# Optimization experiments

Measured on AMD Instinct MI355X. Metric: run time of the kernel, lower is better.

## Reference

```python
import jax, jax.numpy as jnp
import numpy as np

B, DIM, H, W = 32, 384, 32, 32
ORDER = 5
DIMS = [DIM // 2**i for i in range(ORDER)][::-1]  # [24,48,96,192,384]
SUM_DIMS = sum(DIMS)                               # 744 == 2*DIM - DIMS[0]
SCALE = 1.0 / 3.0
EPS = 1e-5


def setup_inputs() -> dict:
    key = jax.random.key(0)
    ks = jax.random.split(key, 32)

    def n(k, shape, s=0.02):
        return jax.random.normal(k, shape, jnp.float32) * s

    inp = {}
    inp['x'] = jax.random.normal(ks[0], (B, DIM, H, W), jnp.float32)
    # norm1: LayerNorm([dim, H, W]) -> per-element affine
    inp['ln1_w'] = jnp.ones((DIM, H, W), jnp.float32) + n(ks[1], (DIM, H, W))
    inp['ln1_b'] = n(ks[2], (DIM, H, W))
    # gnconv params
    inp['proj_in_w'] = n(ks[3], (2 * DIM, DIM))   # 1x1 conv stored as [O,C]
    inp['proj_in_b'] = n(ks[4], (2 * DIM,))
    inp['dw_w'] = n(ks[5], (SUM_DIMS, 1, 7, 7))   # depthwise 7x7
    inp['dw_b'] = n(ks[6], (SUM_DIMS,))
    for i in range(ORDER - 1):
        inp[f'pw{i}_w'] = n(ks[7 + 2 * i], (DIMS[i + 1], DIMS[i]))
        inp[f'pw{i}_b'] = n(ks[8 + 2 * i], (DIMS[i + 1],))
    inp['proj_out_w'] = n(ks[15], (DIM, DIM))
    inp['proj_out_b'] = n(ks[16], (DIM,))
    # norm2 + MLP
    inp['ln2_w'] = jnp.ones((DIM,), jnp.float32) + n(ks[17], (DIM,))
    inp['ln2_b'] = n(ks[18], (DIM,))
    inp['fc1_w'] = n(ks[19], (4 * DIM, DIM))
    inp['fc1_b'] = n(ks[20], (4 * DIM,))
    inp['fc2_w'] = n(ks[21], (DIM, 4 * DIM))
    inp['fc2_b'] = n(ks[22], (DIM,))
    # layer scales
    inp['gamma1'] = 1e-6 * jnp.ones((DIM,), jnp.float32)
    inp['gamma2'] = 1e-6 * jnp.ones((DIM,), jnp.float32)
    return inp


def _conv1x1(x, w, b):
    # x: [B,C,H,W], w: [O,C] -> [B,O,H,W]
    return jnp.einsum('bchw,oc->bohw', x, w) + b[None, :, None, None]


def _dwconv7(x, w, b):
    y = jax.lax.conv_general_dilated(
        x, w, window_strides=(1, 1), padding=[(3, 3), (3, 3)],
        dimension_numbers=('NCHW', 'OIHW', 'NCHW'),
        feature_group_count=x.shape[1])
    return y + b[None, :, None, None]


def reference(x, ln1_w, ln1_b, proj_in_w, proj_in_b, dw_w, dw_b,
              pw0_w, pw0_b, pw1_w, pw1_b, pw2_w, pw2_b, pw3_w, pw3_b,
              proj_out_w, proj_out_b, ln2_w, ln2_b,
              fc1_w, fc1_b, fc2_w, fc2_b, gamma1, gamma2):
    # ---- norm1: LayerNorm over (C,H,W) jointly ----
    mu = x.mean(axis=(1, 2, 3), keepdims=True)
    var = x.var(axis=(1, 2, 3), keepdims=True)
    h = (x - mu) * jax.lax.rsqrt(var + EPS) * ln1_w[None] + ln1_b[None]

    # ---- gnconv (recursive gated conv) ----
    fused = _conv1x1(h, proj_in_w, proj_in_b)          # [B, 2*DIM, H, W]
    pwa = fused[:, :DIMS[0]]
    abc = fused[:, DIMS[0]:]                            # [B, SUM_DIMS, H, W]
    dw = _dwconv7(abc, dw_w, dw_b) * SCALE
    dw_list = jnp.split(dw, np.cumsum(DIMS)[:-1].tolist(), axis=1)
    y = pwa * dw_list[0]
    for i, (wp, bp) in enumerate([(pw0_w, pw0_b), (pw1_w, pw1_b), (pw2_w, pw2_b), (pw3_w, pw3_b)]):
        y = _conv1x1(y, wp, bp) * dw_list[i + 1]
    y = _conv1x1(y, proj_out_w, proj_out_b)             # [B, DIM, H, W]

    x = x + gamma1[None, :, None, None] * y             # residual 1 (drop_path=0 -> identity)

    # ---- ConvNeXt-style MLP, channels-last ----
    h = jnp.transpose(x, (0, 2, 3, 1))                  # [B,H,W,C]
    mu2 = h.mean(axis=-1, keepdims=True)
    var2 = h.var(axis=-1, keepdims=True)
    h = (h - mu2) * jax.lax.rsqrt(var2 + EPS) * ln2_w + ln2_b
    h = jnp.einsum('bhwc,oc->bhwo', h, fc1_w) + fc1_b
    h = jax.nn.gelu(h, approximate=False)               # torch GELU default = erf
    h = jnp.einsum('bhwc,oc->bhwo', h, fc2_w) + fc2_b
    h = gamma2 * h
    h = jnp.transpose(h, (0, 3, 1, 2))                  # back to NCHW
    return x + h
```

## Files before the change

### kernel.cpp

```cpp
#include <hip/hip_runtime.h>
#include <math.h>

#define HW 1024
#define CDIM 384
#define NB 32
#define MTOT (NB * HW)
#define EPS 1e-5f

typedef unsigned short u16;
typedef short s8v __attribute__((ext_vector_type(8)));
typedef float f4v __attribute__((ext_vector_type(4)));

union U8 { s8v v; u16 u[8]; };

__device__ __forceinline__ float bf2f(u16 u) {
  union { float f; unsigned int i; } x; x.i = ((unsigned int)u) << 16; return x.f;
}
__device__ __forceinline__ u16 f2bf(float f) {
  union { float f; unsigned int i; } x; x.f = f;
  unsigned int r = (x.i + 0x7FFFu + ((x.i >> 16) & 1u)) >> 16;
  return (u16)r;
}
__device__ __forceinline__ float gelu_exact(float v) {
  return 0.5f * v * (1.f + erff(v * 0.70710678118654752f));
}

__device__ __forceinline__ void gload16(const u16* g, u16* l) {
  __builtin_amdgcn_global_load_lds(
      (const __attribute__((address_space(1))) unsigned int*)(unsigned long long)(const void*)g,
      (__attribute__((address_space(3))) unsigned int*)(unsigned int)(unsigned long long)(void*)l,
      16, 0, 0);
}

__global__ __launch_bounds__(256) void k_statsA(const float* __restrict__ x,
                                                float* __restrict__ part) {
  int blk = blockIdx.x;
  const float4* xb = (const float4*)(x + (size_t)blk * 12288);
  float s = 0.f, s2 = 0.f;
  for (int i = threadIdx.x; i < 3072; i += 256) {
    float4 v = xb[i];
    s += v.x + v.y + v.z + v.w;
    s2 += v.x * v.x + v.y * v.y + v.z * v.z + v.w * v.w;
  }
  __shared__ float ls[256], ls2[256];
  ls[threadIdx.x] = s; ls2[threadIdx.x] = s2;
  __syncthreads();
  for (int off = 128; off > 0; off >>= 1) {
    if (threadIdx.x < off) {
      ls[threadIdx.x] += ls[threadIdx.x + off];
      ls2[threadIdx.x] += ls2[threadIdx.x + off];
    }
    __syncthreads();
  }
  if (threadIdx.x == 0) { part[blk * 2] = ls[0]; part[blk * 2 + 1] = ls2[0]; }
}

__global__ void k_statsB(const float* __restrict__ part, float* __restrict__ stats) {
  int b = threadIdx.x;
  if (b >= 32) return;
  float s = 0.f, s2 = 0.f;
  for (int i = 0; i < 32; i++) {
    s += part[(b * 32 + i) * 2];
    s2 += part[(b * 32 + i) * 2 + 1];
  }
  const float inv_n = 1.f / (CDIM * HW);
  float m = s * inv_n;
  stats[b] = m;
  stats[32 + b] = rsqrtf(s2 * inv_n - m * m + EPS);
}

__global__ __launch_bounds__(256) void k_cvtwE(const float* __restrict__ piw,
                                               const float* __restrict__ pow_,
                                               const float* __restrict__ p0w,
                                               const float* __restrict__ p1w,
                                               const float* __restrict__ p2w,
                                               const float* __restrict__ p3w,
                                               u16* __restrict__ dst) {
  int i = blockIdx.x * 256 + threadIdx.x;
  if (i < 294912) dst[i] = f2bf(piw[i]);
  else if (i < 442368) dst[i] = f2bf(pow_[i - 294912]);
  else if (i < 443904) { int j = i - 442368, o = j >> 5, k = j & 31;
    dst[i] = (k < 24) ? f2bf(p0w[o * 24 + k]) : (u16)0; }
  else if (i < 450048) { int j = i - 443904, o = j >> 6, k = j & 63;
    dst[i] = (k < 48) ? f2bf(p1w[o * 48 + k]) : (u16)0; }
  else if (i < 468480) dst[i] = f2bf(p2w[i - 450048]);
  else dst[i] = f2bf(p3w[i - 468480]);
}

__global__ __launch_bounds__(256) void k_cvtwL(const float* __restrict__ fc1,
                                               const float* __restrict__ fc2,
                                               u16* __restrict__ dst) {
  int i = blockIdx.x * 256 + threadIdx.x;
  if (i < 589824) dst[i] = f2bf(fc1[i]);
  else dst[i] = f2bf(fc2[i - 589824]);
}

__global__ __launch_bounds__(256) void k_trln1(const float* __restrict__ x,
                                               const float* __restrict__ lnw,
                                               const float* __restrict__ lnb,
                                               const float* __restrict__ stats,
                                               u16* __restrict__ xn,
                                               u16* __restrict__ hn) {
  int pt = blockIdx.x, ct = blockIdx.y, b = blockIdx.z;
  __shared__ float xs[32][33], hs[32][33];
  float m = stats[b], rs = stats[32 + b];
  int t = threadIdx.x;
  int ci0 = t >> 5, pi = t & 31;
#pragma unroll
  for (int it = 0; it < 4; it++) {
    int ci = ci0 + it * 8;
    int c = ct * 32 + ci;
    size_t src = ((size_t)b * CDIM + c) * HW + pt * 32 + pi;
    size_t wsrc = (size_t)c * HW + pt * 32 + pi;
    float xv = x[src];
    xs[ci][pi] = xv;
    hs[ci][pi] = (xv - m) * rs * lnw[wsrc] + lnb[wsrc];
  }
  __syncthreads();
  int co = t & 31, pr0 = t >> 5;
#pragma unroll
  for (int it = 0; it < 4; it++) {
    int pr = pr0 + it * 8;
    int p = pt * 32 + pr;
    int c = ct * 32 + co;
    size_t dst = ((size_t)b * HW + p) * CDIM + c;
    xn[dst] = f2bf(xs[co][pr]);
    hn[dst] = f2bf(hs[co][pr]);
  }
}

template <int MODE>
__global__ __launch_bounds__(256)
void k_mfma(const u16* __restrict__ A, const u16* __restrict__ Wb,
            const float* __restrict__ bias, void* __restrict__ Out,
            const u16* __restrict__ gate, int gate_off,
            const u16* __restrict__ resbf, const float* __restrict__ gvec,
            int m_base, int K, int O, int OS) {
  __shared__ u16 As[4096];
  __shared__ u16 Bs[4096];
  const int t = threadIdx.x;
  const int m0 = blockIdx.x * 128, o0 = blockIdx.y * 128;
  const int w = t >> 6, l = t & 63;
  const int wm = (w >> 1) * 64, wn = (w & 1) * 64;
  const int lr = l & 15, lk = (l >> 4) * 8;

  const u16* gA = A + (size_t)(m0 + w * 32 + (l >> 2)) * K + (l & 3) * 8;
  const u16* gB = Wb + (size_t)(o0 + w * 32 + (l >> 2)) * K + (l & 3) * 8;
  u16* ldsA0 = As + w * 1024;
  u16* ldsB0 = Bs + w * 1024;

  f4v acc[4][4];
#pragma unroll
  for (int i = 0; i < 4; i++)
#pragma unroll
    for (int j = 0; j < 4; j++) acc[i][j] = {};

  for (int k0 = 0; k0 < K; k0 += 32) {
    gload16(gA + k0, ldsA0);
    gload16(gA + 16 * K + k0, ldsA0 + 512);
    gload16(gB + k0, ldsB0);
    gload16(gB + 16 * K + k0, ldsB0 + 512);
    __syncthreads();
    s8v a[4], b[4];
#pragma unroll
    for (int mi = 0; mi < 4; mi++)
      a[mi] = *(const s8v*)&As[(wm + mi * 16 + lr) * 32 + lk];
#pragma unroll
    for (int fj = 0; fj < 4; fj++)
      b[fj] = *(const s8v*)&Bs[(wn + fj * 16 + lr) * 32 + lk];
#pragma unroll
    for (int mi = 0; mi < 4; mi++)
#pragma unroll
      for (int fj = 0; fj < 4; fj++)
        acc[mi][fj] = __builtin_amdgcn_mfma_f32_16x16x32_bf16(a[mi], b[fj], acc[mi][fj], 0, 0, 0);
    __syncthreads();
  }

  const int orow = (l >> 4) * 4;
#pragma unroll
  for (int mi = 0; mi < 4; mi++) {
    int p = m0 + wm + mi * 16 + orow;
#pragma unroll
    for (int fj = 0; fj < 4; fj++) {
      int o = o0 + wn + fj * 16 + lr;
      if (MODE == 1 && o >= OS) continue;
      float bo = (MODE == 1 && o >= O) ? 0.f : bias[o];
      float gv = (MODE == 2 || MODE == 4) ? gvec[o] : 0.f;
      if (MODE == 4) {
        int gp = m_base + p;
        float4 st;
        float* stp = &st.x;
#pragma unroll
        for (int r = 0; r < 4; r++)
          stp[r] = bf2f(resbf[(size_t)(gp + r) * CDIM + o]) + gv * (acc[mi][fj][r] + bo);
        int bb = gp >> 10, hw = gp & 1023;
        *(float4*)((float*)Out + ((size_t)bb * CDIM + o) * HW + hw) = st;
      } else {
#pragma unroll
        for (int r = 0; r < 4; r++) {
          float val = acc[mi][fj][r] + bo;
          size_t rowi = (size_t)(p + r);
          if (MODE == 0) {
            ((u16*)Out)[rowi * OS + o] = f2bf(val);
          } else if (MODE == 1) {
            float g = (o < O) ? bf2f(gate[rowi * 744 + gate_off + o]) : 0.f;
            ((u16*)Out)[rowi * OS + o] = (o < O) ? f2bf(val * g) : (u16)0;
          } else if (MODE == 2) {
            size_t idx = rowi * CDIM + o;
            ((u16*)Out)[idx] = f2bf(bf2f(resbf[idx]) + gv * val);
          } else if (MODE == 3) {
            ((u16*)Out)[rowi * OS + o] = f2bf(gelu_exact(val));
          }
        }
      }
    }
  }
}

template <int MODE>
__global__ __launch_bounds__(256)
void k_mfma64(const u16* __restrict__ A, const u16* __restrict__ Wb,
              const float* __restrict__ bias, void* __restrict__ Out,
              const u16* __restrict__ gate, int gate_off,
              const u16* __restrict__ resbf, const float* __restrict__ gvec,
              int m_base, int K, int O, int OS) {
  __shared__ u16 As[4096];
  __shared__ u16 Bs[2048];
  const int t = threadIdx.x;
  const int m0 = blockIdx.x * 128, o0 = blockIdx.y * 64;
  const int w = t >> 6, l = t & 63;
  const int wm = w * 32;
  const int lr = l & 15, lk = (l >> 4) * 8;

  const u16* gA = A + (size_t)(m0 + w * 32 + (l >> 2)) * K + (l & 3) * 8;
  const u16* gB = Wb + (size_t)(o0 + w * 16 + (l >> 2)) * K + (l & 3) * 8;
  u16* ldsA0 = As + w * 1024;
  u16* ldsB0 = Bs + w * 512;

  f4v acc[2][4];
#pragma unroll
  for (int i = 0; i < 2; i++)
#pragma unroll
    for (int j = 0; j < 4; j++) acc[i][j] = {};

  for (int k0 = 0; k0 < K; k0 += 32) {
    gload16(gA + k0, ldsA0);
    gload16(gA + 16 * K + k0, ldsA0 + 512);
    gload16(gB + k0, ldsB0);
    __syncthreads();
    s8v a[2], b[4];
#pragma unroll
    for (int mi = 0; mi < 2; mi++)
      a[mi] = *(const s8v*)&As[(wm + mi * 16 + lr) * 32 + lk];
#pragma unroll
    for (int fj = 0; fj < 4; fj++)
      b[fj] = *(const s8v*)&Bs[(fj * 16 + lr) * 32 + lk];
#pragma unroll
    for (int mi = 0; mi < 2; mi++)
#pragma unroll
      for (int fj = 0; fj < 4; fj++)
        acc[mi][fj] = __builtin_amdgcn_mfma_f32_16x16x32_bf16(a[mi], b[fj], acc[mi][fj], 0, 0, 0);
    __syncthreads();
  }

  const int orow = (l >> 4) * 4;
#pragma unroll
  for (int mi = 0; mi < 2; mi++) {
    int p = m0 + wm + mi * 16 + orow;
#pragma unroll
    for (int fj = 0; fj < 4; fj++) {
      int o = o0 + fj * 16 + lr;
      if (MODE == 1 && o >= OS) continue;
      float bo = (MODE == 1 && o >= O) ? 0.f : bias[o];
      float gv = (MODE == 2 || MODE == 4) ? gvec[o] : 0.f;
      if (MODE == 4) {
        int gp = m_base + p;
        float4 st;
        float* stp = &st.x;
#pragma unroll
        for (int r = 0; r < 4; r++)
          stp[r] = bf2f(resbf[(size_t)(gp + r) * CDIM + o]) + gv * (acc[mi][fj][r] + bo);
        int bb = gp >> 10, hw = gp & 1023;
        *(float4*)((float*)Out + ((size_t)bb * CDIM + o) * HW + hw) = st;
      } else {
#pragma unroll
        for (int r = 0; r < 4; r++) {
          float val = acc[mi][fj][r] + bo;
          size_t rowi = (size_t)(p + r);
          if (MODE == 0) {
            ((u16*)Out)[rowi * OS + o] = f2bf(val);
          } else if (MODE == 1) {
            float g = (o < O) ? bf2f(gate[rowi * 744 + gate_off + o]) : 0.f;
            ((u16*)Out)[rowi * OS + o] = (o < O) ? f2bf(val * g) : (u16)0;
          } else if (MODE == 2) {
            size_t idx = rowi * CDIM + o;
            ((u16*)Out)[idx] = f2bf(bf2f(resbf[idx]) + gv * val);
          } else if (MODE == 3) {
            ((u16*)Out)[rowi * OS + o] = f2bf(gelu_exact(val));
          }
        }
      }
    }
  }
}

__global__ __launch_bounds__(256) void k_dwconv(const u16* __restrict__ fused,
                                                const float* __restrict__ w,
                                                const float* __restrict__ bias,
                                                u16* __restrict__ dwo) {
  const int ys = blockIdx.x;
  const int cb = blockIdx.y;
  const int b = blockIdx.z;
  __shared__ u16 tile[10][32][64];
  __shared__ float wk[64][49];
  const int c0 = cb * 64;
  const int t = threadIdx.x;
  for (int i = t; i < 64 * 64; i += 256) {
    int k = i >> 6, cc = i & 63;
    if (k < 49) wk[cc][k] = (c0 + cc < 744) ? w[(size_t)(c0 + cc) * 49 + k] : 0.f;
  }
  const int lx = t >> 3, lco = (t & 7) * 8;
  const int fch = 24 + c0 + lco;
#pragma unroll
  for (int yy = 0; yy < 10; yy++) {
    int y = ys * 4 - 3 + yy;
    s8v v = {0, 0, 0, 0, 0, 0, 0, 0};
    if (y >= 0 && y < 32 && fch < 768)
      v = *(const s8v*)(fused + ((size_t)b * HW + y * 32 + lx) * 768 + fch);
    *(s8v*)&tile[yy][lx][lco] = v;
  }
  __syncthreads();
  const int c = t & 63, dy = t >> 6;
  const bool valid = (c0 + c) < 744;
  const float bv = valid ? bias[c0 + c] : 0.f;
  float acc[32];
#pragma unroll
  for (int x = 0; x < 32; x++) acc[x] = 0.f;
#pragma unroll
  for (int ky = 0; ky < 7; ky++) {
    int yy = dy + ky;
    float r[38];
    r[0] = r[1] = r[2] = 0.f; r[35] = r[36] = r[37] = 0.f;
#pragma unroll
    for (int x = 0; x < 32; x++) r[x + 3] = bf2f(tile[yy][x][c]);
#pragma unroll
    for (int kx = 0; kx < 7; kx++) {
      float wv = wk[c][ky * 7 + kx];
#pragma unroll
      for (int x = 0; x < 32; x++) acc[x] += r[x + kx] * wv;
    }
  }
  if (valid) {
    const int yout = ys * 4 + dy;
    const size_t prow = (size_t)b * HW + yout * 32;
#pragma unroll
    for (int x = 0; x < 32; x++)
      dwo[(prow + x) * 744 + c0 + c] = f2bf((acc[x] + bv) * (1.f / 3.f));
  }
}

__global__ __launch_bounds__(256) void k_y0(const u16* __restrict__ fused,
                                            const u16* __restrict__ dwo,
                                            u16* __restrict__ y0) {
  int i = blockIdx.x * 256 + threadIdx.x;
  int p = i >> 5, c = i & 31;
  y0[i] = (c < 24) ? f2bf(bf2f(fused[(size_t)p * 768 + c]) * bf2f(dwo[(size_t)p * 744 + c]))
                   : (u16)0;
}

__global__ __launch_bounds__(256) void k_ln2(const u16* __restrict__ xm,
                                             const float* __restrict__ w,
                                             const float* __restrict__ bb,
                                             u16* __restrict__ outp) {
  int row = blockIdx.x * 4 + (threadIdx.x >> 6);
  int l = threadIdx.x & 63;
  float v[8];
  float s = 0.f, s2 = 0.f;
  if (l < 48) {
    U8 u;
    u.v = *(const s8v*)(xm + (size_t)row * CDIM + l * 8);
#pragma unroll
    for (int i = 0; i < 8; i++) {
      v[i] = bf2f(u.u[i]);
      s += v[i]; s2 += v[i] * v[i];
    }
  }
#pragma unroll
  for (int off = 32; off > 0; off >>= 1) {
    s += __shfl_xor(s, off);
    s2 += __shfl_xor(s2, off);
  }
  const float inv_n = 1.f / CDIM;
  float m = s * inv_n;
  float rs = rsqrtf(s2 * inv_n - m * m + EPS);
  if (l < 48) {
    U8 res;
#pragma unroll
    for (int i = 0; i < 8; i++) {
      int c = l * 8 + i;
      res.u[i] = f2bf((v[i] - m) * rs * w[c] + bb[c]);
    }
    *(s8v*)(outp + (size_t)row * CDIM + l * 8) = res.v;
  }
}

extern "C" void kernel_launch(void* const* d_in, const int* in_sizes, int n_in,
                              void* d_out, int out_size, void* d_ws, size_t ws_size,
                              hipStream_t stream) {
  const float* x          = (const float*)d_in[0];
  const float* ln1_w      = (const float*)d_in[1];
  const float* ln1_b      = (const float*)d_in[2];
  const float* proj_in_w  = (const float*)d_in[3];
  const float* proj_in_b  = (const float*)d_in[4];
  const float* dw_w       = (const float*)d_in[5];
  const float* dw_b       = (const float*)d_in[6];
  const float* pw0_w      = (const float*)d_in[7];
  const float* pw0_b      = (const float*)d_in[8];
  const float* pw1_w      = (const float*)d_in[9];
  const float* pw1_b      = (const float*)d_in[10];
  const float* pw2_w      = (const float*)d_in[11];
  const float* pw2_b      = (const float*)d_in[12];
  const float* pw3_w      = (const float*)d_in[13];
  const float* pw3_b      = (const float*)d_in[14];
  const float* proj_out_w = (const float*)d_in[15];
  const float* proj_out_b = (const float*)d_in[16];
  const float* ln2_w      = (const float*)d_in[17];
  const float* ln2_b      = (const float*)d_in[18];
  const float* fc1_w      = (const float*)d_in[19];
  const float* fc1_b      = (const float*)d_in[20];
  const float* fc2_w      = (const float*)d_in[21];
  const float* fc2_b      = (const float*)d_in[22];
  const float* gamma1     = (const float*)d_in[23];
  const float* gamma2     = (const float*)d_in[24];
  float* out = (float*)d_out;

  const size_t MiB = 1ull << 20;
  char* ws = (char*)d_ws;
  u16* xn   = (u16*)(ws + 0);
  u16* hn   = (u16*)(ws + 24 * MiB);
  u16* fus  = (u16*)(ws + 48 * MiB);
  u16* dw   = (u16*)(ws + 96 * MiB);
  u16* wE   = (u16*)(ws + 142 * MiB + 512 * 1024);
  float* stats = (float*)(ws + 143 * MiB + 768 * 1024);
  float* part  = stats + 64;
  u16* y0 = (u16*)(ws + 24 * MiB);
  u16* y1 = (u16*)(ws + 26 * MiB);
  u16* y2 = (u16*)(ws + 30 * MiB);
  u16* y3 = (u16*)(ws + 36 * MiB);
  u16* y4 = (u16*)(ws + 48 * MiB);
  u16* xmid = (u16*)(ws + 72 * MiB);
  u16* ln2h = (u16*)(ws + 0);
  u16* fc1b = (u16*)(ws + 24 * MiB);
  u16* fc2b = fc1b + 589824;
  u16* h1 = (u16*)(ws + 96 * MiB);

  u16* piw_b = wE;
  u16* pow_b = wE + 294912;
  u16* pw0b  = wE + 442368;
  u16* pw1b  = wE + 443904;
  u16* pw2b  = wE + 450048;
  u16* pw3b  = wE + 468480;

  k_statsA<<<1024, 256, 0, stream>>>(x, part);
  k_statsB<<<1, 64, 0, stream>>>(part, stats);
  k_cvtwE<<<2118, 256, 0, stream>>>(proj_in_w, proj_out_w, pw0_w, pw1_w, pw2_w, pw3_w, wE);
  k_trln1<<<dim3(32, 12, NB), 256, 0, stream>>>(x, ln1_w, ln1_b, stats, xn, hn);
  k_mfma<0><<<dim3(256, 6), 256, 0, stream>>>(hn, piw_b, proj_in_b, fus, nullptr, 0,
                                              nullptr, nullptr, 0, 384, 768, 768);
  k_dwconv<<<dim3(8, 12, NB), 256, 0, stream>>>(fus, dw_w, dw_b, dw);
  k_y0<<<(MTOT * 32) / 256, 256, 0, stream>>>(fus, dw, y0);
  k_mfma64<1><<<dim3(256, 1), 256, 0, stream>>>(y0, pw0b, pw0_b, y1, dw, 24, nullptr,
                                                nullptr, 0, 32, 48, 64);
  k_mfma64<1><<<dim3(256, 2), 256, 0, stream>>>(y1, pw1b, pw1_b, y2, dw, 72, nullptr,
                                                nullptr, 0, 64, 96, 96);
  k_mfma64<1><<<dim3(256, 3), 256, 0, stream>>>(y2, pw2b, pw2_b, y3, dw, 168, nullptr,
                                                nullptr, 0, 96, 192, 192);
  k_mfma64<1><<<dim3(256, 6), 256, 0, stream>>>(y3, pw3b, pw3_b, y4, dw, 360, nullptr,
                                                nullptr, 0, 192, 384, 384);
  k_mfma64<2><<<dim3(256, 6), 256, 0, stream>>>(y4, pow_b, proj_out_b, xmid, nullptr, 0,
                                                xn, gamma1, 0, 384, 384, 384);
  k_ln2<<<MTOT / 4, 256, 0, stream>>>(xmid, ln2_w, ln2_b, ln2h);
  k_cvtwL<<<4608, 256, 0, stream>>>(fc1_w, fc2_w, fc1b);
  for (int ch = 0; ch < 2; ch++) {
    int m_base = ch * 16384;
    k_mfma<3><<<dim3(128, 12), 256, 0, stream>>>(ln2h + (size_t)m_base * CDIM, fc1b,
                                                 fc1_b, h1, nullptr, 0, nullptr, nullptr,
                                                 0, 384, 1536, 1536);
    k_mfma64<4><<<dim3(128, 6), 256, 0, stream>>>(h1, fc2b, fc2_b, out, nullptr, 0, xmid,
                                                  gamma2, m_base, 1536, 384, 384);
  }
}
```

Measured before the change: 388.0 us.

## Double-buffer LDS tiles in MFMA GEMM kernels to overlap loads with compute

Both GEMM kernels now prefetch the next K-slice of A and B into a second shared-memory buffer while MFMAs run on the current one. This removes one barrier per K step. The aim is to hide global load latency behind matrix math. It doubles LDS use per block, which may lower occupancy, and it relies on the end-of-loop barrier to order the async loads.

Result: faster. 377.5 us, median of 2 (-2.7%).

```diff
diff --git a/kernel.cpp b/kernel.cpp
--- a/kernel.cpp
+++ b/kernel.cpp
@@ -136,8 +136,8 @@
             const u16* __restrict__ gate, int gate_off,
             const u16* __restrict__ resbf, const float* __restrict__ gvec,
             int m_base, int K, int O, int OS) {
-  __shared__ u16 As[4096];
-  __shared__ u16 Bs[4096];
+  __shared__ u16 As[8192];
+  __shared__ u16 Bs[8192];
   const int t = threadIdx.x;
   const int m0 = blockIdx.x * 128, o0 = blockIdx.y * 128;
   const int w = t >> 6, l = t & 63;
@@ -155,25 +155,36 @@
 #pragma unroll
     for (int j = 0; j < 4; j++) acc[i][j] = {};
 
+  gload16(gA, ldsA0);
+  gload16(gA + 16 * K, ldsA0 + 512);
+  gload16(gB, ldsB0);
+  gload16(gB + 16 * K, ldsB0 + 512);
+  __syncthreads();
+
+  int cur = 0;
   for (int k0 = 0; k0 < K; k0 += 32) {
-    gload16(gA + k0, ldsA0);
-    gload16(gA + 16 * K + k0, ldsA0 + 512);
-    gload16(gB + k0, ldsB0);
-    gload16(gB + 16 * K + k0, ldsB0 + 512);
-    __syncthreads();
+    if (k0 + 32 < K) {
+      const int nx = (cur ^ 1) * 4096;
+      gload16(gA + k0 + 32, ldsA0 + nx);
+      gload16(gA + 16 * K + k0 + 32, ldsA0 + nx + 512);
+      gload16(gB + k0 + 32, ldsB0 + nx);
+      gload16(gB + 16 * K + k0 + 32, ldsB0 + nx + 512);
+    }
+    const int cb = cur * 4096;
     s8v a[4], b[4];
 #pragma unroll
     for (int mi = 0; mi < 4; mi++)
-      a[mi] = *(const s8v*)&As[(wm + mi * 16 + lr) * 32 + lk];
+      a[mi] = *(const s8v*)&As[cb + (wm + mi * 16 + lr) * 32 + lk];
 #pragma unroll
     for (int fj = 0; fj < 4; fj++)
-      b[fj] = *(const s8v*)&Bs[(wn + fj * 16 + lr) * 32 + lk];
+      b[fj] = *(const s8v*)&Bs[cb + (wn + fj * 16 + lr) * 32 + lk];
 #pragma unroll
     for (int mi = 0; mi < 4; mi++)
 #pragma unroll
       for (int fj = 0; fj < 4; fj++)
         acc[mi][fj] = __builtin_amdgcn_mfma_f32_16x16x32_bf16(a[mi], b[fj], acc[mi][fj], 0, 0, 0);
     __syncthreads();
+    cur ^= 1;
   }
 
   const int orow = (l >> 4) * 4;
@@ -224,8 +235,8 @@
               const u16* __restrict__ gate, int gate_off,
               const u16* __restrict__ resbf, const float* __restrict__ gvec,
               int m_base, int K, int O, int OS) {
-  __shared__ u16 As[4096];
-  __shared__ u16 Bs[2048];
+  __shared__ u16 As[8192];
+  __shared__ u16 Bs[4096];
   const int t = threadIdx.x;
   const int m0 = blockIdx.x * 128, o0 = blockIdx.y * 64;
   const int w = t >> 6, l = t & 63;
@@ -243,24 +254,33 @@
 #pragma unroll
     for (int j = 0; j < 4; j++) acc[i][j] = {};
 
+  gload16(gA, ldsA0);
+  gload16(gA + 16 * K, ldsA0 + 512);
+  gload16(gB, ldsB0);
+  __syncthreads();
+
+  int cur = 0;
   for (int k0 = 0; k0 < K; k0 += 32) {
-    gload16(gA + k0, ldsA0);
-    gload16(gA + 16 * K + k0, ldsA0 + 512);
-    gload16(gB + k0, ldsB0);
-    __syncthreads();
+    if (k0 + 32 < K) {
+      gload16(gA + k0 + 32, ldsA0 + (cur ^ 1) * 4096);
+      gload16(gA + 16 * K + k0 + 32, ldsA0 + (cur ^ 1) * 4096 + 512);
+      gload16(gB + k0 + 32, ldsB0 + (cur ^ 1) * 2048);
+    }
+    const int cbA = cur * 4096, cbB = cur * 2048;
     s8v a[2], b[4];
 #pragma unroll
     for (int mi = 0; mi < 2; mi++)
-      a[mi] = *(const s8v*)&As[(wm + mi * 16 + lr) * 32 + lk];
+      a[mi] = *(const s8v*)&As[cbA + (wm + mi * 16 + lr) * 32 + lk];
 #pragma unroll
     for (int fj = 0; fj < 4; fj++)
-      b[fj] = *(const s8v*)&Bs[(fj * 16 + lr) * 32 + lk];
+      b[fj] = *(const s8v*)&Bs[cbB + (fj * 16 + lr) * 32 + lk];
 #pragma unroll
     for (int mi = 0; mi < 2; mi++)
 #pragma unroll
       for (int fj = 0; fj < 4; fj++)
         acc[mi][fj] = __builtin_amdgcn_mfma_f32_16x16x32_bf16(a[mi], b[fj], acc[mi][fj], 0, 0, 0);
     __syncthreads();
+    cur ^= 1;
   }
 
   const int orow = (l >> 4) * 4;
```
